# Performance work log

Measured on AMD Instinct MI355X. Metric: run time of the kernel, lower is better.

Reference implementation:

```python
import jax, jax.numpy as jnp
import numpy as np

# Tree: 64 leaves (16 feat -> 16 out), 8 mids (16 feat + 8*16 child = 144 -> 32 out),
# root (16 feat + 8*32 child = 272 -> 64 out), head -> 10 tasks. Eval-mode BatchNorm.
B = 16384
EPS = 1e-5


def setup_inputs() -> dict:
    key = jax.random.key(0)
    ks = jax.random.split(key, 24)
    rn = lambda k, s: jax.random.normal(k, s, dtype=jnp.float32)
    ru = lambda k, s: jax.random.uniform(k, s, dtype=jnp.float32)
    return {
        "x": rn(ks[0], (B, 1168)),
        # leaf layers (64 nodes, 16 -> 16)
        "Wl": rn(ks[1], (64, 16, 16)) * 0.1, "bl": rn(ks[2], (64, 16)) * 0.1,
        "gl": ru(ks[3], (64, 16)) + 0.5, "betal": rn(ks[4], (64, 16)) * 0.1,
        "ml": rn(ks[5], (64, 16)) * 0.1, "vl": ru(ks[6], (64, 16)) + 0.5,
        # mid layers (8 nodes, 144 -> 32)
        "Wm": rn(ks[7], (8, 144, 32)) * 0.1, "bm": rn(ks[8], (8, 32)) * 0.1,
        "gm": ru(ks[9], (8, 32)) + 0.5, "betam": rn(ks[10], (8, 32)) * 0.1,
        "mm": rn(ks[11], (8, 32)) * 0.1, "vm": ru(ks[12], (8, 32)) + 0.5,
        # root layer (272 -> 64)
        "Wr": rn(ks[13], (272, 64)) * 0.1, "br": rn(ks[14], (64,)) * 0.1,
        "gr": ru(ks[15], (64,)) + 0.5, "betar": rn(ks[16], (64,)) * 0.1,
        "mr": rn(ks[17], (64,)) * 0.1, "vr": ru(ks[18], (64,)) + 0.5,
        # root prediction head (64 -> 10 tasks)
        "Wh": rn(ks[19], (64, 10)) * 0.1, "bh": rn(ks[20], (10,)) * 0.1,
    }


def _bn(h, g, b, m, v):
    return (h - m) * jax.lax.rsqrt(v + EPS) * g + b


def reference(x, Wl, bl, gl, betal, ml, vl, Wm, bm, gm, betam, mm, vm,
              Wr, br, gr, betar, mr, vr, Wh, bh):
    n = x.shape[0]
    # leaves: gather own features (contiguous layout), Linear+BN+Tanh, batched over 64 nodes
    xl = x[:, :1024].reshape(n, 64, 16)
    hl = jnp.tanh(_bn(jnp.einsum('bli,lio->blo', xl, Wl) + bl, gl, betal, ml, vl))
    # mids: concat own features with 8 leaf-child outputs -> [n, 8, 144]
    xm = x[:, 1024:1152].reshape(n, 8, 16)
    mid_in = jnp.concatenate([xm, hl.reshape(n, 8, 128)], axis=-1)
    hm = jnp.tanh(_bn(jnp.einsum('bmi,mio->bmo', mid_in, Wm) + bm, gm, betam, mm, vm))
    # root: concat own features with 8 mid outputs -> [n, 272]
    root_in = jnp.concatenate([x[:, 1152:1168], hm.reshape(n, 256)], axis=-1)
    hr = jnp.tanh(_bn(root_in @ Wr + br, gr, betar, mr, vr))
    # root prediction head (eval-mode forward returns only root prediction)
    return hr @ Wh + bh
```

## Files before the change

kernel.cpp:

```cpp
#include <hip/hip_runtime.h>

typedef __attribute__((ext_vector_type(8))) short bf16x8;
typedef __attribute__((ext_vector_type(4))) float f32x4;

#define EPS 1e-5f
#define K2L 2.8853900817779268f

#define N_FRAG_BLOCKS 182
#define WSB_LEAF 0
#define WSB_MID  64
#define WSB_ROOT 144
#define WSB_HEAD 180
#define ST_SL 0
#define ST_TL 1024
#define ST_SM 2048
#define ST_TM 2304
#define ST_SR 2560
#define ST_TR 2624
#define WS_ST_BYTE_OFF (N_FRAG_BLOCKS * 1024)

__device__ __forceinline__ unsigned short f2bf(float f) {
    unsigned u = __float_as_uint(f);
    unsigned r = u + 0x7fffu + ((u >> 16) & 1u);
    return (unsigned short)(r >> 16);
}

__device__ __forceinline__ unsigned pack2bf(float a, float b) {
    return (unsigned)f2bf(a) | ((unsigned)f2bf(b) << 16);
}

__device__ __forceinline__ bf16x8 pack8(float4 a, float4 b) {
    union { unsigned u[4]; bf16x8 v; } r;
    r.u[0] = pack2bf(a.x, a.y); r.u[1] = pack2bf(a.z, a.w);
    r.u[2] = pack2bf(b.x, b.y); r.u[3] = pack2bf(b.z, b.w);
    return r.v;
}

__device__ __forceinline__ float bn_act(float acc, float Sp, float Tp) {
    float e = exp2f(fmaf(acc, Sp, Tp));
    float r = __builtin_amdgcn_rcpf(e + 1.0f);
    return fmaf(-2.0f, r, 1.0f);
}

__global__ void ontology_prep(
    const float* __restrict__ Wl, const float* __restrict__ Wm,
    const float* __restrict__ Wr, const float* __restrict__ Wh,
    const float* __restrict__ bl, const float* __restrict__ gl,
    const float* __restrict__ betal, const float* __restrict__ ml,
    const float* __restrict__ vl,
    const float* __restrict__ bm, const float* __restrict__ gm,
    const float* __restrict__ betam, const float* __restrict__ mm,
    const float* __restrict__ vm,
    const float* __restrict__ br, const float* __restrict__ gr,
    const float* __restrict__ betar, const float* __restrict__ mr,
    const float* __restrict__ vr,
    unsigned short* __restrict__ wsFrag, float* __restrict__ wsST)
{
    const int b = blockIdx.x;
    const int t = threadIdx.x;
    if (b < N_FRAG_BLOCKS) {
        const int row = t & 15, g = t >> 4;
        unsigned short vals[8];
        #pragma unroll
        for (int i = 0; i < 8; ++i) {
            const int k = g * 8 + i;
            float v = 0.f;
            if (b < 64) {
                const int l = b;
                if ((l & 1) == 0) { if (k < 16)  v = Wl[l * 256 + k * 16 + row]; }
                else              { if (k >= 16) v = Wl[l * 256 + (k - 16) * 16 + row]; }
            } else if (b < 144) {
                const int idx = b - 64, m = idx / 10, rem = idx % 10;
                const int tt = rem / 5, s = rem % 5;
                const int krow = s * 32 + k;
                if (krow < 144) v = Wm[m * 4608 + krow * 32 + tt * 16 + row];
            } else if (b < 180) {
                const int idx = b - 144, tt = idx / 9, s = idx % 9;
                if (s == 0) { if (k < 16) v = Wr[k * 64 + tt * 16 + row]; }
                else { const int krow = 16 + (s - 1) * 32 + k;
                       v = Wr[krow * 64 + tt * 16 + row]; }
            } else {
                const int s = b - 180, krow = s * 32 + k;
                if (row < 10) v = Wh[krow * 10 + row];
            }
            vals[i] = f2bf(v);
        }
        #pragma unroll
        for (int i = 0; i < 8; ++i) wsFrag[b * 512 + t * 8 + i] = vals[i];
    } else if (b == N_FRAG_BLOCKS) {
        for (int i = 0; i < 16; ++i) {
            const int id = t + 64 * i;
            const float S = gl[id] * rsqrtf(vl[id] + EPS);
            wsST[ST_SL + id] = S * K2L;
            wsST[ST_TL + id] = ((bl[id] - ml[id]) * S + betal[id]) * K2L;
        }
    } else if (b == N_FRAG_BLOCKS + 1) {
        for (int i = 0; i < 4; ++i) {
            const int id = t + 64 * i;
            const float S = gm[id] * rsqrtf(vm[id] + EPS);
            wsST[ST_SM + id] = S * K2L;
            wsST[ST_TM + id] = ((bm[id] - mm[id]) * S + betam[id]) * K2L;
        }
    } else {
        const int id = t;
        const float S = gr[id] * rsqrtf(vr[id] + EPS);
        wsST[ST_SR + id] = S * K2L;
        wsST[ST_TR + id] = ((br[id] - mr[id]) * S + betar[id]) * K2L;
    }
}

__global__ __launch_bounds__(256, 4) void ontology_mfma(
    const float* __restrict__ x,
    const unsigned short* __restrict__ wsFrag,
    const float* __restrict__ wsST,
    const float* __restrict__ bh,
    float* __restrict__ out)
{
    __shared__ __align__(16) unsigned short mid_in[4][16][168];
    __shared__ __align__(16) unsigned short hm[4][16][40];
    __shared__ __align__(16) float slab[4][16][34];
    unsigned short (*hr)[72] = (unsigned short (*)[72])&mid_in[0][0][0];

    const int tid  = threadIdx.x;
    const int w    = tid >> 6;
    const int lane = tid & 63;
    const int c    = lane & 15;
    const int g    = lane >> 4;
    const int rowbase = blockIdx.x * 16;
    const float* xrow = x + (size_t)(rowbase + c) * 1168;

    const float* Sl = wsST + ST_SL; const float* Tl = wsST + ST_TL;
    const float* Sm = wsST + ST_SM; const float* Tm = wsST + ST_TM;
    const float* Sr = wsST + ST_SR; const float* Tr = wsST + ST_TR;

    { uint2 z; z.x = 0u; z.y = 0u; *(uint2*)&mid_in[w][c][144 + 4 * g] = z; }

    f32x4 accR[4];
    #pragma unroll
    for (int t = 0; t < 4; ++t) { f32x4 z0 = {0.f,0.f,0.f,0.f}; accR[t] = z0; }

    if (w == 3) {
        const float* rp = xrow + 1152 + (g & 1) * 8;
        bf16x8 bfrag = pack8(*(const float4*)rp, *(const float4*)(rp + 4));
        #pragma unroll
        for (int t = 0; t < 4; ++t) {
            bf16x8 a = *(const bf16x8*)(wsFrag + (WSB_ROOT + t * 9) * 512 + lane * 8);
            accR[t] = __builtin_amdgcn_mfma_f32_16x16x32_bf16(a, bfrag, accR[t], 0, 0, 0);
        }
    }

    #pragma unroll
    for (int it = 0; it < 2; ++it) {
        const int M = w + 4 * it;
        float4 xm4 = *(const float4*)(xrow + 1024 + M * 16 + 4 * g);
        float4 xp[4][2];
        #pragma unroll
        for (int p = 0; p < 4; ++p) {
            const float* a = xrow + (M * 4 + p) * 32 + g * 8;
            xp[p][0] = *(const float4*)a;
            xp[p][1] = *(const float4*)(a + 4);
        }
        bf16x8 lfr[8];
        #pragma unroll
        for (int l = 0; l < 8; ++l)
            lfr[l] = *(const bf16x8*)(wsFrag + (WSB_LEAF + M * 8 + l) * 512 + lane * 8);
        { uint2 pm; pm.x = pack2bf(xm4.x, xm4.y); pm.y = pack2bf(xm4.z, xm4.w);
          *(uint2*)&mid_in[w][c][4 * g] = pm; }
        #pragma unroll
        for (int p = 0; p < 4; ++p) {
            bf16x8 bfrag = pack8(xp[p][0], xp[p][1]);
            #pragma unroll
            for (int e = 0; e < 2; ++e) {
                const int l = 2 * p + e, leaf = M * 8 + l;
                f32x4 zz = {0.f,0.f,0.f,0.f};
                f32x4 acc = __builtin_amdgcn_mfma_f32_16x16x32_bf16(lfr[l], bfrag, zz, 0, 0, 0);
                const int po = leaf * 16 + 4 * g;
                float4 S = *(const float4*)(Sl + po);
                float4 T = *(const float4*)(Tl + po);
                float h0 = bn_act(acc[0], S.x, T.x);
                float h1 = bn_act(acc[1], S.y, T.y);
                float h2 = bn_act(acc[2], S.z, T.z);
                float h3 = bn_act(acc[3], S.w, T.w);
                uint2 pk; pk.x = pack2bf(h0, h1); pk.y = pack2bf(h2, h3);
                *(uint2*)&mid_in[w][c][16 + l * 16 + 4 * g] = pk;
            }
        }
        #pragma unroll
        for (int tt = 0; tt < 2; ++tt) {
            f32x4 acc = {0.f,0.f,0.f,0.f};
            const unsigned short* fb = wsFrag + (WSB_MID + M * 10 + tt * 5) * 512 + lane * 8;
            #pragma unroll
            for (int s = 0; s < 5; ++s) {
                bf16x8 bfrag = *(const bf16x8*)&mid_in[w][c][s * 32 + g * 8];
                bf16x8 a0 = *(const bf16x8*)(fb + s * 512);
                acc = __builtin_amdgcn_mfma_f32_16x16x32_bf16(a0, bfrag, acc, 0, 0, 0);
            }
            const int po = M * 32 + tt * 16 + 4 * g;
            float4 S = *(const float4*)(Sm + po);
            float4 T = *(const float4*)(Tm + po);
            float h0 = bn_act(acc[0], S.x, T.x);
            float h1 = bn_act(acc[1], S.y, T.y);
            float h2 = bn_act(acc[2], S.z, T.z);
            float h3 = bn_act(acc[3], S.w, T.w);
            uint2 pk; pk.x = pack2bf(h0, h1); pk.y = pack2bf(h2, h3);
            *(uint2*)&hm[w][c][tt * 16 + 4 * g] = pk;
        }
        {
            bf16x8 bfrag = *(const bf16x8*)&hm[w][c][g * 8];
            #pragma unroll
            for (int t = 0; t < 4; ++t) {
                bf16x8 a = *(const bf16x8*)(wsFrag + (WSB_ROOT + t * 9 + M + 1) * 512 + lane * 8);
                accR[t] = __builtin_amdgcn_mfma_f32_16x16x32_bf16(a, bfrag, accR[t], 0, 0, 0);
            }
        }
    }

    #pragma unroll
    for (int t = 0; t < 2; ++t) {
        float2 lo; lo.x = accR[t][0]; lo.y = accR[t][1];
        float2 hi; hi.x = accR[t][2]; hi.y = accR[t][3];
        *(float2*)&slab[w][c][t * 16 + 4 * g]     = lo;
        *(float2*)&slab[w][c][t * 16 + 4 * g + 2] = hi;
    }
    asm volatile("s_waitcnt lgkmcnt(0)" ::: "memory");
    __builtin_amdgcn_s_barrier();
    if (w < 2) {
        float4 sum = {0.f,0.f,0.f,0.f};
        #pragma unroll
        for (int v = 0; v < 4; ++v) {
            float2 lo = *(const float2*)&slab[v][c][w * 16 + 4 * g];
            float2 hi = *(const float2*)&slab[v][c][w * 16 + 4 * g + 2];
            sum.x += lo.x; sum.y += lo.y; sum.z += hi.x; sum.w += hi.y;
        }
        const int po = w * 16 + 4 * g;
        float4 S = *(const float4*)(Sr + po);
        float4 T = *(const float4*)(Tr + po);
        uint2 pk;
        pk.x = pack2bf(bn_act(sum.x, S.x, T.x), bn_act(sum.y, S.y, T.y));
        pk.y = pack2bf(bn_act(sum.z, S.z, T.z), bn_act(sum.w, S.w, T.w));
        *(uint2*)&hr[c][po] = pk;
    }
    asm volatile("s_waitcnt lgkmcnt(0)" ::: "memory");
    __builtin_amdgcn_s_barrier();

    #pragma unroll
    for (int t = 2; t < 4; ++t) {
        float2 lo; lo.x = accR[t][0]; lo.y = accR[t][1];
        float2 hi; hi.x = accR[t][2]; hi.y = accR[t][3];
        *(float2*)&slab[w][c][(t - 2) * 16 + 4 * g]     = lo;
        *(float2*)&slab[w][c][(t - 2) * 16 + 4 * g + 2] = hi;
    }
    asm volatile("s_waitcnt lgkmcnt(0)" ::: "memory");
    __builtin_amdgcn_s_barrier();
    if (w >= 2) {
        float4 sum = {0.f,0.f,0.f,0.f};
        #pragma unroll
        for (int v = 0; v < 4; ++v) {
            float2 lo = *(const float2*)&slab[v][c][(w - 2) * 16 + 4 * g];
            float2 hi = *(const float2*)&slab[v][c][(w - 2) * 16 + 4 * g + 2];
            sum.x += lo.x; sum.y += lo.y; sum.z += hi.x; sum.w += hi.y;
        }
        const int po = w * 16 + 4 * g;
        float4 S = *(const float4*)(Sr + po);
        float4 T = *(const float4*)(Tr + po);
        uint2 pk;
        pk.x = pack2bf(bn_act(sum.x, S.x, T.x), bn_act(sum.y, S.y, T.y));
        pk.y = pack2bf(bn_act(sum.z, S.z, T.z), bn_act(sum.w, S.w, T.w));
        *(uint2*)&hr[c][po] = pk;
    }
    asm volatile("s_waitcnt lgkmcnt(0)" ::: "memory");
    __builtin_amdgcn_s_barrier();

    if (w == 0) {
        f32x4 acc = {0.f,0.f,0.f,0.f};
        #pragma unroll
        for (int s = 0; s < 2; ++s) {
            bf16x8 bfrag = *(const bf16x8*)&hr[c][s * 32 + g * 8];
            bf16x8 a0 = *(const bf16x8*)(wsFrag + (WSB_HEAD + s) * 512 + lane * 8);
            acc = __builtin_amdgcn_mfma_f32_16x16x32_bf16(a0, bfrag, acc, 0, 0, 0);
        }
        float* op = out + (size_t)(rowbase + c) * 10 + 4 * g;
        if (g < 2) {
            float2 o1 = {acc[0] + bh[4 * g],     acc[1] + bh[4 * g + 1]};
            float2 o2 = {acc[2] + bh[4 * g + 2], acc[3] + bh[4 * g + 3]};
            *(float2*)op = o1;
            *(float2*)(op + 2) = o2;
        } else if (g == 2) {
            float2 o1 = {acc[0] + bh[8], acc[1] + bh[9]};
            *(float2*)op = o1;
        }
    }
}

extern "C" void kernel_launch(void* const* d_in, const int* in_sizes, int n_in,
                              void* d_out, int out_size, void* d_ws, size_t ws_size,
                              hipStream_t stream) {
    const float* x     = (const float*)d_in[0];
    const float* Wl    = (const float*)d_in[1];
    const float* bl    = (const float*)d_in[2];
    const float* gl    = (const float*)d_in[3];
    const float* betal = (const float*)d_in[4];
    const float* ml    = (const float*)d_in[5];
    const float* vl    = (const float*)d_in[6];
    const float* Wm    = (const float*)d_in[7];
    const float* bm    = (const float*)d_in[8];
    const float* gm    = (const float*)d_in[9];
    const float* betam = (const float*)d_in[10];
    const float* mm    = (const float*)d_in[11];
    const float* vm    = (const float*)d_in[12];
    const float* Wr    = (const float*)d_in[13];
    const float* br    = (const float*)d_in[14];
    const float* gr    = (const float*)d_in[15];
    const float* betar = (const float*)d_in[16];
    const float* mr    = (const float*)d_in[17];
    const float* vr    = (const float*)d_in[18];
    const float* Wh    = (const float*)d_in[19];
    const float* bh    = (const float*)d_in[20];
    float* out = (float*)d_out;

    unsigned short* wsFrag = (unsigned short*)d_ws;
    float* wsST = (float*)((char*)d_ws + WS_ST_BYTE_OFF);

    ontology_prep<<<N_FRAG_BLOCKS + 3, 64, 0, stream>>>(
        Wl, Wm, Wr, Wh, bl, gl, betal, ml, vl, bm, gm, betam, mm, vm,
        br, gr, betar, mr, vr, wsFrag, wsST);

    const int n = in_sizes[0] / 1168;
    ontology_mfma<<<n / 16, 256, 0, stream>>>(x, wsFrag, wsST, bh, out);
}
```

Before: 31.61 us.

## Prefetch second mid group's x loads and use hardware bf16 pack conversion

Replaces the software round-to-nearest bf16 packing with the v_cvt_pk_bf16_f32 instruction, cutting ALU work in every conversion. Also unrolls the two mid-node iterations manually, issuing the global loads for the second group's features before the first group's compute and deferring the root-feature MFMA, so the second group's memory latency overlaps the first group's work. Leaf weight fragments are now loaded per MFMA instead of all eight up front. This raises register pressure from the prefetched float4 data, which could lower occupancy.

After: 36.95 us. +16.9%, slower.

```diff
diff --git a/kernel.cpp b/kernel.cpp
--- a/kernel.cpp
+++ b/kernel.cpp
@@ -25,14 +25,16 @@
     return (unsigned short)(r >> 16);
 }
 
-__device__ __forceinline__ unsigned pack2bf(float a, float b) {
-    return (unsigned)f2bf(a) | ((unsigned)f2bf(b) << 16);
+__device__ __forceinline__ unsigned cvt_pk(float a, float b) {
+    unsigned r;
+    asm("v_cvt_pk_bf16_f32 %0, %1, %2" : "=v"(r) : "v"(a), "v"(b));
+    return r;
 }
 
 __device__ __forceinline__ bf16x8 pack8(float4 a, float4 b) {
     union { unsigned u[4]; bf16x8 v; } r;
-    r.u[0] = pack2bf(a.x, a.y); r.u[1] = pack2bf(a.z, a.w);
-    r.u[2] = pack2bf(b.x, b.y); r.u[3] = pack2bf(b.z, b.w);
+    r.u[0] = cvt_pk(a.x, a.y); r.u[1] = cvt_pk(a.z, a.w);
+    r.u[2] = cvt_pk(b.x, b.y); r.u[3] = cvt_pk(b.z, b.w);
     return r.v;
 }
 
@@ -133,85 +135,143 @@
     const float* Sm = wsST + ST_SM; const float* Tm = wsST + ST_TM;
     const float* Sr = wsST + ST_SR; const float* Tr = wsST + ST_TR;
 
-    { uint2 z; z.x = 0u; z.y = 0u; *(uint2*)&mid_in[w][c][144 + 4 * g] = z; }
-
-    f32x4 accR[4];
-    #pragma unroll
-    for (int t = 0; t < 4; ++t) { f32x4 z0 = {0.f,0.f,0.f,0.f}; accR[t] = z0; }
-
+    const int M0 = w, M1 = w + 4;
+
+    float4 xmA = *(const float4*)(xrow + 1024 + M0 * 16 + 4 * g);
+    float4 xpA[4][2];
+    #pragma unroll
+    for (int p = 0; p < 4; ++p) {
+        const float* a = xrow + (M0 * 4 + p) * 32 + g * 8;
+        xpA[p][0] = *(const float4*)a;
+        xpA[p][1] = *(const float4*)(a + 4);
+    }
+    float4 xrA, xrB;
     if (w == 3) {
         const float* rp = xrow + 1152 + (g & 1) * 8;
-        bf16x8 bfrag = pack8(*(const float4*)rp, *(const float4*)(rp + 4));
+        xrA = *(const float4*)rp;
+        xrB = *(const float4*)(rp + 4);
+    }
+
+    { uint2 z; z.x = 0u; z.y = 0u; *(uint2*)&mid_in[w][c][144 + 4 * g] = z; }
+
+    f32x4 accR[4];
+    #pragma unroll
+    for (int t = 0; t < 4; ++t) { f32x4 z0 = {0.f,0.f,0.f,0.f}; accR[t] = z0; }
+
+    bf16x8 bfA[4];
+    #pragma unroll
+    for (int p = 0; p < 4; ++p) bfA[p] = pack8(xpA[p][0], xpA[p][1]);
+    { uint2 pm; pm.x = cvt_pk(xmA.x, xmA.y); pm.y = cvt_pk(xmA.z, xmA.w);
+      *(uint2*)&mid_in[w][c][4 * g] = pm; }
+
+    float4 xmB = *(const float4*)(xrow + 1024 + M1 * 16 + 4 * g);
+    float4 xpB[4][2];
+    #pragma unroll
+    for (int p = 0; p < 4; ++p) {
+        const float* a = xrow + (M1 * 4 + p) * 32 + g * 8;
+        xpB[p][0] = *(const float4*)a;
+        xpB[p][1] = *(const float4*)(a + 4);
+    }
+
+    #pragma unroll
+    for (int p = 0; p < 4; ++p) {
+        #pragma unroll
+        for (int e = 0; e < 2; ++e) {
+            const int l = 2 * p + e, leaf = M0 * 8 + l;
+            bf16x8 afrag = *(const bf16x8*)(wsFrag + (WSB_LEAF + leaf) * 512 + lane * 8);
+            f32x4 zz = {0.f,0.f,0.f,0.f};
+            f32x4 acc = __builtin_amdgcn_mfma_f32_16x16x32_bf16(afrag, bfA[p], zz, 0, 0, 0);
+            const int po = leaf * 16 + 4 * g;
+            float4 S = *(const float4*)(Sl + po);
+            float4 T = *(const float4*)(Tl + po);
+            uint2 pk;
+            pk.x = cvt_pk(bn_act(acc[0], S.x, T.x), bn_act(acc[1], S.y, T.y));
+            pk.y = cvt_pk(bn_act(acc[2], S.z, T.z), bn_act(acc[3], S.w, T.w));
+            *(uint2*)&mid_in[w][c][16 + l * 16 + 4 * g] = pk;
+        }
+    }
+    #pragma unroll
+    for (int tt = 0; tt < 2; ++tt) {
+        f32x4 acc = {0.f,0.f,0.f,0.f};
+        const unsigned short* fb = wsFrag + (WSB_MID + M0 * 10 + tt * 5) * 512 + lane * 8;
+        #pragma unroll
+        for (int s = 0; s < 5; ++s) {
+            bf16x8 bfrag = *(const bf16x8*)&mid_in[w][c][s * 32 + g * 8];
+            bf16x8 a0 = *(const bf16x8*)(fb + s * 512);
+            acc = __builtin_amdgcn_mfma_f32_16x16x32_bf16(a0, bfrag, acc, 0, 0, 0);
+        }
+        const int po = M0 * 32 + tt * 16 + 4 * g;
+        float4 S = *(const float4*)(Sm + po);
+        float4 T = *(const float4*)(Tm + po);
+        uint2 pk;
+        pk.x = cvt_pk(bn_act(acc[0], S.x, T.x), bn_act(acc[1], S.y, T.y));
+        pk.y = cvt_pk(bn_act(acc[2], S.z, T.z), bn_act(acc[3], S.w, T.w));
+        *(uint2*)&hm[w][c][tt * 16 + 4 * g] = pk;
+    }
+    {
+        bf16x8 bfrag = *(const bf16x8*)&hm[w][c][g * 8];
+        #pragma unroll
+        for (int t = 0; t < 4; ++t) {
+            bf16x8 a = *(const bf16x8*)(wsFrag + (WSB_ROOT + t * 9 + M0 + 1) * 512 + lane * 8);
+            accR[t] = __builtin_amdgcn_mfma_f32_16x16x32_bf16(a, bfrag, accR[t], 0, 0, 0);
+        }
+    }
+
+    bf16x8 bfB[4];
+    #pragma unroll
+    for (int p = 0; p < 4; ++p) bfB[p] = pack8(xpB[p][0], xpB[p][1]);
+    { uint2 pm; pm.x = cvt_pk(xmB.x, xmB.y); pm.y = cvt_pk(xmB.z, xmB.w);
+      *(uint2*)&mid_in[w][c][4 * g] = pm; }
+    #pragma unroll
+    for (int p = 0; p < 4; ++p) {
+        #pragma unroll
+        for (int e = 0; e < 2; ++e) {
+            const int l = 2 * p + e, leaf = M1 * 8 + l;
+            bf16x8 afrag = *(const bf16x8*)(wsFrag + (WSB_LEAF + leaf) * 512 + lane * 8);
+            f32x4 zz = {0.f,0.f,0.f,0.f};
+            f32x4 acc = __builtin_amdgcn_mfma_f32_16x16x32_bf16(afrag, bfB[p], zz, 0, 0, 0);
+            const int po = leaf * 16 + 4 * g;
+            float4 S = *(const float4*)(Sl + po);
+            float4 T = *(const float4*)(Tl + po);
+            uint2 pk;
+            pk.x = cvt_pk(bn_act(acc[0], S.x, T.x), bn_act(acc[1], S.y, T.y));
+            pk.y = cvt_pk(bn_act(acc[2], S.z, T.z), bn_act(acc[3], S.w, T.w));
+            *(uint2*)&mid_in[w][c][16 + l * 16 + 4 * g] = pk;
+        }
+    }
+    #pragma unroll
+    for (int tt = 0; tt < 2; ++tt) {
+        f32x4 acc = {0.f,0.f,0.f,0.f};
+        const unsigned short* fb = wsFrag + (WSB_MID + M1 * 10 + tt * 5) * 512 + lane * 8;
+        #pragma unroll
+        for (int s = 0; s < 5; ++s) {
+            bf16x8 bfrag = *(const bf16x8*)&mid_in[w][c][s * 32 + g * 8];
+            bf16x8 a0 = *(const bf16x8*)(fb + s * 512);
+            acc = __builtin_amdgcn_mfma_f32_16x16x32_bf16(a0, bfrag, acc, 0, 0, 0);
+        }
+        const int po = M1 * 32 + tt * 16 + 4 * g;
+        float4 S = *(const float4*)(Sm + po);
+        float4 T = *(const float4*)(Tm + po);
+        uint2 pk;
+        pk.x = cvt_pk(bn_act(acc[0], S.x, T.x), bn_act(acc[1], S.y, T.y));
+        pk.y = cvt_pk(bn_act(acc[2], S.z, T.z), bn_act(acc[3], S.w, T.w));
+        *(uint2*)&hm[w][c][tt * 16 + 4 * g] = pk;
+    }
+    {
+        bf16x8 bfrag = *(const bf16x8*)&hm[w][c][g * 8];
+        #pragma unroll
+        for (int t = 0; t < 4; ++t) {
+            bf16x8 a = *(const bf16x8*)(wsFrag + (WSB_ROOT + t * 9 + M1 + 1) * 512 + lane * 8);
+            accR[t] = __builtin_amdgcn_mfma_f32_16x16x32_bf16(a, bfrag, accR[t], 0, 0, 0);
+        }
+    }
+
+    if (w == 3) {
+        bf16x8 bfrag = pack8(xrA, xrB);
         #pragma unroll
         for (int t = 0; t < 4; ++t) {
             bf16x8 a = *(const bf16x8*)(wsFrag + (WSB_ROOT + t * 9) * 512 + lane * 8);
             accR[t] = __builtin_amdgcn_mfma_f32_16x16x32_bf16(a, bfrag, accR[t], 0, 0, 0);
-        }
-    }
-
-    #pragma unroll
-    for (int it = 0; it < 2; ++it) {
-        const int M = w + 4 * it;
-        float4 xm4 = *(const float4*)(xrow + 1024 + M * 16 + 4 * g);
-        float4 xp[4][2];
-        #pragma unroll
-        for (int p = 0; p < 4; ++p) {
-            const float* a = xrow + (M * 4 + p) * 32 + g * 8;
-            xp[p][0] = *(const float4*)a;
-            xp[p][1] = *(const float4*)(a + 4);
-        }
-        bf16x8 lfr[8];
-        #pragma unroll
-        for (int l = 0; l < 8; ++l)
-            lfr[l] = *(const bf16x8*)(wsFrag + (WSB_LEAF + M * 8 + l) * 512 + lane * 8);
-        { uint2 pm; pm.x = pack2bf(xm4.x, xm4.y); pm.y = pack2bf(xm4.z, xm4.w);
-          *(uint2*)&mid_in[w][c][4 * g] = pm; }
-        #pragma unroll
-        for (int p = 0; p < 4; ++p) {
-            bf16x8 bfrag = pack8(xp[p][0], xp[p][1]);
-            #pragma unroll
-            for (int e = 0; e < 2; ++e) {
-                const int l = 2 * p + e, leaf = M * 8 + l;
-                f32x4 zz = {0.f,0.f,0.f,0.f};
-                f32x4 acc = __builtin_amdgcn_mfma_f32_16x16x32_bf16(lfr[l], bfrag, zz, 0, 0, 0);
-                const int po = leaf * 16 + 4 * g;
-                float4 S = *(const float4*)(Sl + po);
-                float4 T = *(const float4*)(Tl + po);
-                float h0 = bn_act(acc[0], S.x, T.x);
-                float h1 = bn_act(acc[1], S.y, T.y);
-                float h2 = bn_act(acc[2], S.z, T.z);
-                float h3 = bn_act(acc[3], S.w, T.w);
-                uint2 pk; pk.x = pack2bf(h0, h1); pk.y = pack2bf(h2, h3);
-                *(uint2*)&mid_in[w][c][16 + l * 16 + 4 * g] = pk;
-            }
-        }
-        #pragma unroll
-        for (int tt = 0; tt < 2; ++tt) {
-            f32x4 acc = {0.f,0.f,0.f,0.f};
-            const unsigned short* fb = wsFrag + (WSB_MID + M * 10 + tt * 5) * 512 + lane * 8;
-            #pragma unroll
-            for (int s = 0; s < 5; ++s) {
-                bf16x8 bfrag = *(const bf16x8*)&mid_in[w][c][s * 32 + g * 8];
-                bf16x8 a0 = *(const bf16x8*)(fb + s * 512);
-                acc = __builtin_amdgcn_mfma_f32_16x16x32_bf16(a0, bfrag, acc, 0, 0, 0);
-            }
-            const int po = M * 32 + tt * 16 + 4 * g;
-            float4 S = *(const float4*)(Sm + po);
-            float4 T = *(const float4*)(Tm + po);
-            float h0 = bn_act(acc[0], S.x, T.x);
-            float h1 = bn_act(acc[1], S.y, T.y);
-            float h2 = bn_act(acc[2], S.z, T.z);
-            float h3 = bn_act(acc[3], S.w, T.w);
-            uint2 pk; pk.x = pack2bf(h0, h1); pk.y = pack2bf(h2, h3);
-            *(uint2*)&hm[w][c][tt * 16 + 4 * g] = pk;
-        }
-        {
-            bf16x8 bfrag = *(const bf16x8*)&hm[w][c][g * 8];
-            #pragma unroll
-            for (int t = 0; t < 4; ++t) {
-                bf16x8 a = *(const bf16x8*)(wsFrag + (WSB_ROOT + t * 9 + M + 1) * 512 + lane * 8);
-                accR[t] = __builtin_amdgcn_mfma_f32_16x16x32_bf16(a, bfrag, accR[t], 0, 0, 0);
-            }
         }
     }
 
@@ -236,8 +296,8 @@
         float4 S = *(const float4*)(Sr + po);
         float4 T = *(const float4*)(Tr + po);
         uint2 pk;
-        pk.x = pack2bf(bn_act(sum.x, S.x, T.x), bn_act(sum.y, S.y, T.y));
-        pk.y = pack2bf(bn_act(sum.z, S.z, T.z), bn_act(sum.w, S.w, T.w));
+        pk.x = cvt_pk(bn_act(sum.x, S.x, T.x), bn_act(sum.y, S.y, T.y));
+        pk.y = cvt_pk(bn_act(sum.z, S.z, T.z), bn_act(sum.w, S.w, T.w));
         *(uint2*)&hr[c][po] = pk;
     }
     asm volatile("s_waitcnt lgkmcnt(0)" ::: "memory");
@@ -264,8 +324,8 @@
         float4 S = *(const float4*)(Sr + po);
         float4 T = *(const float4*)(Tr + po);
         uint2 pk;
-        pk.x = pack2bf(bn_act(sum.x, S.x, T.x), bn_act(sum.y, S.y, T.y));
-        pk.y = pack2bf(bn_act(sum.z, S.z, T.z), bn_act(sum.w, S.w, T.w));
+        pk.x = cvt_pk(bn_act(sum.x, S.x, T.x), bn_act(sum.y, S.y, T.y));
+        pk.y = cvt_pk(bn_act(sum.z, S.z, T.z), bn_act(sum.w, S.w, T.w));
         *(uint2*)&hr[c][po] = pk;
     }
     asm volatile("s_waitcnt lgkmcnt(0)" ::: "memory");
```
